# Kernel tuning notes

Hardware: AMD Instinct MI355X
Metric: run time of the kernel (lower is better)

Reference implementation:

```python
import jax, jax.numpy as jnp
import numpy as np
from jax import lax

B, L, DDYN, DSTAT, H = 512, 64, 16, 8, 512
N_BANK, C_CAND, K_TOP, N_PROTO = 50000, 1024, 16, 8
T_TARG, Q_QUANT = 2, 3
TEMP = 0.2


def _l2norm(x, eps=1e-12):
    # matches torch.nn.functional.normalize: x / max(||x||, eps)
    n = jnp.sqrt(jnp.sum(x * x, axis=-1, keepdims=True))
    return x / jnp.maximum(n, eps)


def setup_inputs() -> dict:
    key = jax.random.key(0)
    ks = jax.random.split(key, 24)
    s = 0.02
    inp = {
        'sequence_values': jax.random.normal(ks[0], (B, L, DDYN), jnp.float32),
        'sequence_masks': jnp.ones((B, L), jnp.float32),
        'static_values': jax.random.normal(ks[1], (B, DSTAT), jnp.float32),
        'bank_keys': jax.random.normal(ks[2], (N_BANK, H), jnp.float32),
        'bank_values': jax.random.normal(ks[3], (N_BANK, H), jnp.float32),
        'candidate_indices': jax.random.randint(ks[4], (B, C_CAND), 0, N_BANK, jnp.int64),
        # encoder params (SequenceEncoder stand-in: masked-mean + linear + relu)
        'W_seq': jax.random.normal(ks[5], (DDYN, H), jnp.float32) * s,
        'W_stat': jax.random.normal(ks[6], (DSTAT, H), jnp.float32) * s,
        'b_enc': jnp.zeros((H,), jnp.float32),
        # retrieval / prototype / fusion params
        'W_q': jax.random.normal(ks[7], (H, H), jnp.float32) * s,
        'b_q': jnp.zeros((H,), jnp.float32),
        'prototype_tokens': jax.random.normal(ks[8], (N_PROTO, H), jnp.float32) * 0.02,
        'W_tr': jax.random.normal(ks[9], (2 * H, H), jnp.float32) * s,
        'b_tr': jnp.zeros((H,), jnp.float32),
        'W_gate': jax.random.normal(ks[10], (3 * H, H), jnp.float32) * s,
        'b_gate': jnp.zeros((H,), jnp.float32),
        'W_out': jax.random.normal(ks[11], (H, H), jnp.float32) * s,
        'b_out': jnp.zeros((H,), jnp.float32),
        # per-target heads stacked: [T, H, Q] and [T, H]
        'W_quant': jax.random.normal(ks[12], (T_TARG, H, Q_QUANT), jnp.float32) * s,
        'b_quant': jnp.zeros((T_TARG, Q_QUANT), jnp.float32),
        'W_ev': jax.random.normal(ks[13], (T_TARG, H), jnp.float32) * s,
        'b_ev': jnp.zeros((T_TARG,), jnp.float32),
    }
    return inp


def reference(sequence_values, sequence_masks, static_values, bank_keys, bank_values,
              candidate_indices, W_seq, W_stat, b_enc, W_q, b_q, prototype_tokens,
              W_tr, b_tr, W_gate, b_gate, W_out, b_out, W_quant, b_quant, W_ev, b_ev):
    # --- encoder (masked mean pool + linear + relu stand-in for SequenceEncoder) ---
    m = sequence_masks[..., None]                                   # [B,L,1]
    pooled = (sequence_values * m).sum(1) / jnp.maximum(m.sum(1), 1e-6)
    local_hidden = jax.nn.relu(pooled @ W_seq + static_values @ W_stat + b_enc)  # [B,H]

    # --- normalized query ---
    query = _l2norm(local_hidden @ W_q + b_q)                       # [B,H]

    # --- donor retrieval: gather + dot + topk + softmax + weighted sum ---
    cand_keys = bank_keys[candidate_indices]                        # [B,C,H]
    sim = jnp.einsum('bch,bh->bc', cand_keys, query)                # [B,C]
    top_scores, top_pos = lax.top_k(sim, K_TOP)                     # [B,K]
    weights = jax.nn.softmax(top_scores / max(TEMP, 1e-6), axis=-1)
    sel_idx = jnp.take_along_axis(candidate_indices, top_pos, axis=1)  # [B,K]
    donor_hidden = jnp.einsum('bk,bkh->bh', weights, bank_values[sel_idx])

    # --- prototype attention ---
    protos_n = _l2norm(prototype_tokens)                            # [P,H]
    pw = jax.nn.softmax(query @ protos_n.T, axis=-1)                # [B,P]
    proto_hidden = pw @ prototype_tokens                            # [B,H]

    # --- transfer / gate / fuse (dropout is identity at eval) ---
    transfer = jax.nn.relu(jnp.concatenate([donor_hidden, proto_hidden], -1) @ W_tr + b_tr)
    gate = jax.nn.sigmoid(
        jnp.concatenate([local_hidden, donor_hidden, proto_hidden], -1) @ W_gate + b_gate)
    fused = gate * local_hidden + (1.0 - gate) * transfer
    fused = jax.nn.relu(fused @ W_out + b_out)                      # [B,H]

    # --- heads: sorted quantiles [B,T,Q] and event logits [B,T] ---
    quant = jnp.sort(jnp.einsum('bh,thq->btq', fused, W_quant) + b_quant, axis=-1)
    logit = jnp.einsum('bh,th->bt', fused, W_ev) + b_ev
    return jnp.concatenate([quant.reshape(quant.shape[0], -1), logit], axis=-1)  # [B, T*Q+T]
```

## Files before the change

### kernel.cpp

```cpp
#include <hip/hip_runtime.h>
#include <hip/hip_bf16.h>

typedef __hip_bfloat16 bf16;
typedef float f4v __attribute__((ext_vector_type(4)));
typedef float f2v __attribute__((ext_vector_type(2)));

__device__ __forceinline__ float lo16(unsigned u){ return __uint_as_float(u << 16); }
__device__ __forceinline__ float hi16(unsigned u){ return __uint_as_float(u & 0xffff0000u); }

#define Bn 512
#define Hn 512
#define Cn 1024
#define Kn 16
#define NBANK 50000
#define NIDPAD 50176

__device__ __forceinline__ int clamp_id(int id){
    return (id < 0) ? 0 : ((id >= NBANK) ? (NBANK - 1) : id);
}

#define A_OFF    0
#define B_OFF    262144
#define C_OFF    524288
#define D_OFF    786432
#define SIM_OFF  1048576
#define ELO_OFF  1048576
#define EHI_OFF  1310720
#define F_OFF    1572864
#define G_OFF2   1835008
#define WS_FLOATS 2097152

#define HIST_I   0
#define CURSOR_I NIDPAD
#define GTOT_I   (2*NIDPAD)
#define OFFS_I   (2*NIDPAD + 256)

__global__ __launch_bounds__(256) void k_enc(
    const float* __restrict__ seq, const float* __restrict__ mask, const float* __restrict__ stat,
    const float* __restrict__ W_seq, const float* __restrict__ W_stat, const float* __restrict__ b_enc,
    const int* __restrict__ cand32, float* __restrict__ ws)
{
    const int b = blockIdx.x, t = threadIdx.x;
    const int h0 = 2*t, h1 = 2*t + 1;

    {
        const int c64 = ((cand32[1] | cand32[3] | cand32[5] | cand32[7]) == 0) ? 1 : 0;
        int* hist = (int*)(ws + F_OFF) + HIST_I;
        #pragma unroll
        for (int u = 0; u < 4; u++) {
            int idx = b*Cn + u*256 + t;
            atomicAdd(&hist[clamp_id(cand32[(size_t)idx << c64])], 1);
        }
    }

    __shared__ float s_pool[16], s_stat[8];
    if (t < 16) {
        float acc = 0.f, ms = 0.f;
        for (int l = 0; l < 64; l++) {
            float m = mask[b*64 + l];
            ms  += m;
            acc += seq[(b*64 + l)*16 + t] * m;
        }
        s_pool[t] = acc / fmaxf(ms, 1e-6f);
    } else if (t < 24) {
        s_stat[t - 16] = stat[b*8 + (t - 16)];
    }
    __syncthreads();
    float a0 = b_enc[h0], a1 = b_enc[h1];
    #pragma unroll
    for (int j = 0; j < 16; j++) {
        float2 wv = *(const float2*)(W_seq + j*Hn + h0);
        a0 += s_pool[j]*wv.x; a1 += s_pool[j]*wv.y;
    }
    #pragma unroll
    for (int j = 0; j < 8; j++) {
        float2 wv = *(const float2*)(W_stat + j*Hn + h0);
        a0 += s_stat[j]*wv.x; a1 += s_stat[j]*wv.y;
    }
    float* g = ws + B_OFF + (size_t)b*Hn;
    g[h0] = fmaxf(a0, 0.f); g[h1] = fmaxf(a1, 0.f);
}

__global__ __launch_bounds__(256) void k_scan(
    const int* __restrict__ hist, int* __restrict__ offs, int* __restrict__ gtot)
{
    __shared__ int s[256]; __shared__ int sbase;
    const int t = threadIdx.x, g = blockIdx.x*256 + t;
    const int v = hist[g];
    s[t] = v; __syncthreads();
    #pragma unroll
    for (int off = 1; off < 256; off <<= 1) {
        int x = (t >= off) ? s[t - off] : 0;
        __syncthreads();
        s[t] += x;
        __syncthreads();
    }
    if (t == 255) sbase = atomicAdd(gtot, s[255]);
    __syncthreads();
    offs[g] = sbase + s[t] - v;
}

__global__ __launch_bounds__(256) void k_scatter(
    const int* __restrict__ cand32, int* __restrict__ cursor,
    const int* __restrict__ offs, unsigned* __restrict__ refs)
{
    const int i = blockIdx.x*256 + threadIdx.x;
    const int c64 = ((cand32[1] | cand32[3] | cand32[5] | cand32[7]) == 0) ? 1 : 0;
    const int id = clamp_id(cand32[(size_t)i << c64]);
    const int pos = atomicAdd(&cursor[id], 1);
    refs[offs[id] + pos] = (unsigned)i;
}

__global__ __launch_bounds__(256) void k_qgemm_p(
    const float* __restrict__ W, const float* __restrict__ bias,
    const float* __restrict__ in,
    float* __restrict__ P0, float* __restrict__ P1,
    float* __restrict__ P2, float* __restrict__ P3)
{
    const int ct = blockIdx.x, rt = blockIdx.y, kz = blockIdx.z, t = threadIdx.x;
    __shared__ float lt[64][132];
    {
        int r = t >> 2, c0 = (t & 3)*32;
        const float* src = in + (size_t)(rt*64 + r)*Hn + kz*128 + c0;
        #pragma unroll
        for (int i = 0; i < 8; i++)
            *(float4*)&lt[r][c0 + i*4] = *(const float4*)(src + i*4);
    }
    __syncthreads();
    const int col0 = ct*64 + (t & 15)*4, rbase = (t >> 4)*4;
    float acc[4][4];
    if (kz == 0) {
        float4 bv = *(const float4*)(bias + col0);
        #pragma unroll
        for (int i = 0; i < 4; i++) { acc[i][0]=bv.x; acc[i][1]=bv.y; acc[i][2]=bv.z; acc[i][3]=bv.w; }
    } else {
        #pragma unroll
        for (int i = 0; i < 4; i++) { acc[i][0]=0; acc[i][1]=0; acc[i][2]=0; acc[i][3]=0; }
    }
    const float* wp = W + (size_t)(kz*128)*Hn + col0;
    #pragma unroll 4
    for (int k = 0; k < 128; k++) {
        float4 wv = *(const float4*)(wp + (size_t)k*Hn);
        #pragma unroll
        for (int i = 0; i < 4; i++) {
            float a = lt[rbase + i][k];
            acc[i][0] += a*wv.x; acc[i][1] += a*wv.y; acc[i][2] += a*wv.z; acc[i][3] += a*wv.w;
        }
    }
    float* outp = (kz == 0) ? P0 : (kz == 1) ? P1 : (kz == 2) ? P2 : P3;
    #pragma unroll
    for (int i = 0; i < 4; i++) {
        float* op = outp + (size_t)(rt*64 + rbase + i)*Hn + col0;
        *(float4*)op = make_float4(acc[i][0], acc[i][1], acc[i][2], acc[i][3]);
    }
}

__global__ __launch_bounds__(256) void k_qnorm(float* __restrict__ ws)
{
    const int b = blockIdx.x*4 + (threadIdx.x >> 6), lane = threadIdx.x & 63;
    const size_t o = (size_t)b*Hn + lane*8;
    const float* p0 = ws + A_OFF   + o;
    const float* p1 = ws + ELO_OFF + o;
    const float* p2 = ws + EHI_OFF + o;
    const float* p3 = ws + G_OFF2  + o;
    float4 qa, qb;
    {
        float4 a0 = *(const float4*)p0, a1 = *(const float4*)p1,
               a2 = *(const float4*)p2, a3 = *(const float4*)p3;
        qa = make_float4(((a0.x+a1.x)+a2.x)+a3.x, ((a0.y+a1.y)+a2.y)+a3.y,
                         ((a0.z+a1.z)+a2.z)+a3.z, ((a0.w+a1.w)+a2.w)+a3.w);
        float4 b0 = *(const float4*)(p0+4), b1 = *(const float4*)(p1+4),
               b2 = *(const float4*)(p2+4), b3 = *(const float4*)(p3+4);
        qb = make_float4(((b0.x+b1.x)+b2.x)+b3.x, ((b0.y+b1.y)+b2.y)+b3.y,
                         ((b0.z+b1.z)+b2.z)+b3.z, ((b0.w+b1.w)+b2.w)+b3.w);
    }
    float ss = qa.x*qa.x + qa.y*qa.y + qa.z*qa.z + qa.w*qa.w
             + qb.x*qb.x + qb.y*qb.y + qb.z*qb.z + qb.w*qb.w;
    #pragma unroll
    for (int o2 = 32; o2; o2 >>= 1) ss += __shfl_xor(ss, o2);
    float inv = 1.f / fmaxf(sqrtf(ss), 1e-12f);
    qa.x *= inv; qa.y *= inv; qa.z *= inv; qa.w *= inv;
    qb.x *= inv; qb.y *= inv; qb.z *= inv; qb.w *= inv;
    float* qr = ws + A_OFF + o;
    *(float4*)qr = qa; *(float4*)(qr + 4) = qb;
}

#define DI_LOAD(R0,R1,R2,R3,A0,Bq0,A1,Bq1,A2,Bq2,A3,Bq3,BASE) do {                       \
    int j0_=(BASE), j1_=(BASE)+1, j2_=(BASE)+2, j3_=(BASE)+3;                            \
    const int m_ = n - 1;                                                                \
    const int c1_ = (j1_ < n), c2_ = (j2_ < n), c3_ = (j3_ < n);                         \
    j0_ = j0_>m_?m_:j0_; j1_ = j1_>m_?m_:j1_; j2_ = j2_>m_?m_:j2_; j3_ = j3_>m_?m_:j3_;  \
    R0 = (j0_<64)?(unsigned)__shfl((int)refv,j0_):__builtin_nontemporal_load(refs+start+j0_); \
    R1 = (j1_<64)?(unsigned)__shfl((int)refv,j1_):__builtin_nontemporal_load(refs+start+j1_); \
    R2 = (j2_<64)?(unsigned)__shfl((int)refv,j2_):__builtin_nontemporal_load(refs+start+j2_); \
    R3 = (j3_<64)?(unsigned)__shfl((int)refv,j3_):__builtin_nontemporal_load(refs+start+j3_); \
    {   const float* q0_ = qbase + (size_t)(R0>>10)*Hn + lane*8;                         \
        A0 = *(const float4*)q0_; Bq0 = *(const float4*)(q0_+4); }                       \
    if (c1_) { const float* q1_ = qbase + (size_t)(R1>>10)*Hn + lane*8;                  \
        A1 = *(const float4*)q1_; Bq1 = *(const float4*)(q1_+4); }                       \
    if (c2_) { const float* q2_ = qbase + (size_t)(R2>>10)*Hn + lane*8;                  \
        A2 = *(const float4*)q2_; Bq2 = *(const float4*)(q2_+4); }                       \
    if (c3_) { const float* q3_ = qbase + (size_t)(R3>>10)*Hn + lane*8;                  \
        A3 = *(const float4*)q3_; Bq3 = *(const float4*)(q3_+4); }                       \
} while(0)

#define DI_COMP(R0,R1,R2,R3,A0,Bq0,A1,Bq1,A2,Bq2,A3,Bq3,BASE) do {                       \
    float s0_ = ka.x*A0.x + ka.y*A0.y + ka.z*A0.z + ka.w*A0.w                            \
              + kb.x*Bq0.x + kb.y*Bq0.y + kb.z*Bq0.z + kb.w*Bq0.w;                       \
    float s1_ = ka.x*A1.x + ka.y*A1.y + ka.z*A1.z + ka.w*A1.w                            \
              + kb.x*Bq1.x + kb.y*Bq1.y + kb.z*Bq1.z + kb.w*Bq1.w;                       \
    float s2_ = ka.x*A2.x + ka.y*A2.y + ka.z*A2.z + ka.w*A2.w                            \
              + kb.x*Bq2.x + kb.y*Bq2.y + kb.z*Bq2.z + kb.w*Bq2.w;                       \
    float s3_ = ka.x*A3.x + ka.y*A3.y + ka.z*A3.z + ka.w*A3.w                            \
              + kb.x*Bq3.x + kb.y*Bq3.y + kb.z*Bq3.z + kb.w*Bq3.w;                       \
    s0_ += __shfl_xor(s0_,32); s1_ += __shfl_xor(s1_,32);                                \
    s2_ += __shfl_xor(s2_,32); s3_ += __shfl_xor(s3_,32);                                \
    s0_ += __shfl_xor(s0_,16); s1_ += __shfl_xor(s1_,16);                                \
    s2_ += __shfl_xor(s2_,16); s3_ += __shfl_xor(s3_,16);                                \
    s0_ += __shfl_xor(s0_, 8); s1_ += __shfl_xor(s1_, 8);                                \
    s2_ += __shfl_xor(s2_, 8); s3_ += __shfl_xor(s3_, 8);                                \
    int d_ = (lane >> 3) & 3;                                                            \
    float t_ = d_==0 ? s0_ : d_==1 ? s1_ : d_==2 ? s2_ : s3_;                            \
    t_ += __shfl_xor(t_, 4); t_ += __shfl_xor(t_, 2); t_ += __shfl_xor(t_, 1);           \
    if ((lane & 7) == 0 && lane < 32) {                                                  \
        int dd_ = lane >> 3;                                                             \
        if ((BASE) + dd_ < n) {                                                          \
            unsigned rs_ = dd_==0 ? R0 : dd_==1 ? R1 : dd_==2 ? R2 : R3;                 \
            simw[rs_] = t_;                                                              \
        }                                                                                \
    }                                                                                    \
} while(0)

__global__ __launch_bounds__(256) void k_dotinv(
    const float* __restrict__ bank_keys, const unsigned* __restrict__ refs,
    const int* __restrict__ offs, const int* __restrict__ cnt,
    float* __restrict__ ws)
{
    const int id = blockIdx.x*4 + (threadIdx.x >> 6);
    const int lane = threadIdx.x & 63;
    const int n = cnt[id];
    if (n <= 0) return;
    const int start = offs[id];

    const float* kp = bank_keys + (size_t)id*Hn + lane*8;
    f4v kav = __builtin_nontemporal_load((const f4v*)kp);
    f4v kbv = __builtin_nontemporal_load((const f4v*)(kp + 4));
    float4 ka = make_float4(kav.x, kav.y, kav.z, kav.w);
    float4 kb = make_float4(kbv.x, kbv.y, kbv.z, kbv.w);
    const unsigned refv = refs[start + (lane < n ? lane : n - 1)];
    const float* qbase = ws + A_OFF;
    float* simw = ws + SIM_OFF;

    unsigned Ar0,Ar1,Ar2,Ar3, Br0=0,Br1=0,Br2=0,Br3=0;
    float4 Aa0,Ab0,Aa1,Ab1,Aa2,Ab2,Aa3,Ab3;
    float4 Ba0,Bb0,Ba1,Bb1,Ba2,Bb2,Ba3,Bb3;
    Aa0=Ab0=Aa1=Ab1=Aa2=Ab2=Aa3=Ab3=make_float4(0.f,0.f,0.f,0.f);
    Ba0=Bb0=Ba1=Bb1=Ba2=Bb2=Ba3=Bb3=make_float4(0.f,0.f,0.f,0.f);

    DI_LOAD(Ar0,Ar1,Ar2,Ar3, Aa0,Ab0,Aa1,Ab1,Aa2,Ab2,Aa3,Ab3, 0);
    for (int base = 0; ; ) {
        if (base + 4 < n) DI_LOAD(Br0,Br1,Br2,Br3, Ba0,Bb0,Ba1,Bb1,Ba2,Bb2,Ba3,Bb3, base + 4);
        DI_COMP(Ar0,Ar1,Ar2,Ar3, Aa0,Ab0,Aa1,Ab1,Aa2,Ab2,Aa3,Ab3, base);
        if (base + 8 < n) DI_LOAD(Ar0,Ar1,Ar2,Ar3, Aa0,Ab0,Aa1,Ab1,Aa2,Ab2,Aa3,Ab3, base + 8);
        DI_COMP(Br0,Br1,Br2,Br3, Ba0,Bb0,Ba1,Bb1,Ba2,Bb2,Ba3,Bb3, base + 4);
        base += 8;
        if (base >= n) break;
    }
}

__global__ __launch_bounds__(256) void k_select(
    const float* __restrict__ bank_values, const int* __restrict__ cand32,
    const float* __restrict__ proto, float* __restrict__ ws)
{
    const int b = blockIdx.x, t = threadIdx.x;
    const int w = t >> 6, lane = t & 63;
    const int h0 = 2*t, h1 = 2*t + 1;
    const int c64 = ((cand32[1] | cand32[3] | cand32[5] | cand32[7]) == 0) ? 1 : 0;

    __shared__ __align__(16) float s_sim[Cn];
    __shared__ float s_bv[4]; __shared__ int s_bi[4];
    __shared__ float s_topv[Kn]; __shared__ int s_sel[Kn];
    __shared__ float s_w[Kn];
    __shared__ float s_score[8], s_pw[8];

    *(float4*)&s_sim[t*4] = *(const float4*)(ws + SIM_OFF + (size_t)b*Cn + t*4);

    const float* qr = ws + A_OFF + (size_t)b*Hn + lane*8;
    float4 qa = *(const float4*)qr, qb = *(const float4*)(qr + 4);
    float qv[8] = {qa.x, qa.y, qa.z, qa.w, qb.x, qb.y, qb.z, qb.w};
    __syncthreads();

    for (int k = 0; k < Kn; k++) {
        float best = -1e30f; int bi = 0x7fffffff;
        for (int i = t; i < Cn; i += 256) {
            float v = s_sim[i];
            if (v > best || (v == best && i < bi)) { best = v; bi = i; }
        }
        #pragma unroll
        for (int o = 32; o; o >>= 1) {
            float ov = __shfl_xor(best, o); int oi = __shfl_xor(bi, o);
            if (ov > best || (ov == best && oi < bi)) { best = ov; bi = oi; }
        }
        if (lane == 0) { s_bv[w] = best; s_bi[w] = bi; }
        __syncthreads();
        if (t == 0) {
            float bv = s_bv[0]; int bbi = s_bi[0];
            for (int x = 1; x < 4; x++)
                if (s_bv[x] > bv || (s_bv[x] == bv && s_bi[x] < bbi)) { bv = s_bv[x]; bbi = s_bi[x]; }
            if (bbi < 0 || bbi >= Cn) bbi = 0;
            s_topv[k] = bv; s_sel[k] = bbi; s_sim[bbi] = -1e30f;
        }
        __syncthreads();
    }

    if (t == 0) {
        float m = s_topv[0];
        float e[Kn], ssum = 0.f;
        for (int k = 0; k < Kn; k++) { e[k] = __expf((s_topv[k] - m) * 5.0f); ssum += e[k]; }
        float inv = 1.f / ssum;
        for (int k = 0; k < Kn; k++) s_w[k] = e[k] * inv;
    }
    for (int p = w; p < 8; p += 4) {
        const float* pp = proto + (size_t)p*Hn + lane*8;
        float4 pa = *(const float4*)pp, pb = *(const float4*)(pp + 4);
        float f[8] = {pa.x, pa.y, pa.z, pa.w, pb.x, pb.y, pb.z, pb.w};
        float dq = 0.f, sq = 0.f;
        #pragma unroll
        for (int i = 0; i < 8; i++) { dq += f[i]*qv[i]; sq += f[i]*f[i]; }
        #pragma unroll
        for (int o = 32; o; o >>= 1) { dq += __shfl_xor(dq, o); sq += __shfl_xor(sq, o); }
        if (lane == 0) s_score[p] = dq / fmaxf(sqrtf(sq), 1e-12f);
    }
    __syncthreads();
    if (t == 0) {
        float m = s_score[0];
        for (int p = 1; p < 8; p++) m = fmaxf(m, s_score[p]);
        float e[8], ssum = 0.f;
        for (int p = 0; p < 8; p++) { e[p] = __expf(s_score[p] - m); ssum += e[p]; }
        float inv = 1.f / ssum;
        for (int p = 0; p < 8; p++) s_pw[p] = e[p] * inv;
    }
    __syncthreads();

    {
        float a0 = 0.f, a1 = 0.f;
        #pragma unroll
        for (int k = 0; k < Kn; k++) {
            int id = clamp_id(cand32[(size_t)(b*Cn + s_sel[k]) << c64]);
            f2v v = __builtin_nontemporal_load((const f2v*)(bank_values + (size_t)id*Hn + h0));
            a0 += s_w[k]*v.x; a1 += s_w[k]*v.y;
        }
        float* gd = ws + C_OFF + (size_t)b*Hn;
        gd[h0] = a0; gd[h1] = a1;
    }
    {
        float a0 = 0.f, a1 = 0.f;
        #pragma unroll
        for (int p = 0; p < 8; p++) {
            float2 v = *(const float2*)(proto + (size_t)p*Hn + h0);
            a0 += s_pw[p]*v.x; a1 += s_pw[p]*v.y;
        }
        float* gp = ws + D_OFF + (size_t)b*Hn;
        gp[h0] = a0; gp[h1] = a1;
    }
}

__global__ __launch_bounds__(256) void k_gatetr_p(
    const float* __restrict__ W_tr, const float* __restrict__ b_tr,
    const float* __restrict__ W_gate, const float* __restrict__ b_gate,
    float* __restrict__ ws)
{
    const int ct = blockIdx.x, rt = blockIdx.y, z = blockIdx.z, t = threadIdx.x;
    const int isGate = (z < 3);
    const int sl = isGate ? z : (z - 3);
    const float* W = isGate ? (W_gate + (size_t)(z*512)*Hn) : (W_tr + (size_t)(sl*512)*Hn);
    const float* slab = ws + B_OFF + (size_t)(isGate ? z : (sl + 1))*262144;
    float* outp = isGate
        ? ((z == 0) ? ws + A_OFF : (z == 1) ? ws + ELO_OFF : ws + EHI_OFF)
        : ((sl == 0) ? ws + F_OFF : ws + G_OFF2);

    __shared__ float lt[32][260];
    const int col0 = ct*128 + (t & 31)*4, rbase = (t >> 5)*4;
    float acc[4][4];
    if (z == 0 || z == 3) {
        const float* bias = isGate ? b_gate : b_tr;
        float4 bv = *(const float4*)(bias + col0);
        #pragma unroll
        for (int i = 0; i < 4; i++) { acc[i][0]=bv.x; acc[i][1]=bv.y; acc[i][2]=bv.z; acc[i][3]=bv.w; }
    } else {
        #pragma unroll
        for (int i = 0; i < 4; i++) { acc[i][0]=0; acc[i][1]=0; acc[i][2]=0; acc[i][3]=0; }
    }

    #pragma unroll
    for (int h = 0; h < 2; h++) {
        if (h) __syncthreads();
        {
            int r = t >> 3, c0 = (t & 7)*32;
            const float* src = slab + (size_t)(rt*32 + r)*Hn + h*256 + c0;
            #pragma unroll
            for (int i = 0; i < 8; i++)
                *(float4*)&lt[r][c0 + i*4] = *(const float4*)(src + i*4);
        }
        __syncthreads();
        const float* wp = W + (size_t)(h*256)*Hn + col0;
        #pragma unroll 4
        for (int k = 0; k < 256; k++) {
            float4 wv = *(const float4*)(wp + (size_t)k*Hn);
            #pragma unroll
            for (int i = 0; i < 4; i++) {
                float a = lt[rbase + i][k];
                acc[i][0] += a*wv.x; acc[i][1] += a*wv.y; acc[i][2] += a*wv.z; acc[i][3] += a*wv.w;
            }
        }
    }
    #pragma unroll
    for (int i = 0; i < 4; i++) {
        float* op = outp + (size_t)(rt*32 + rbase + i)*Hn + col0;
        *(float4*)op = make_float4(acc[i][0], acc[i][1], acc[i][2], acc[i][3]);
    }
}

__global__ __launch_bounds__(256) void k_f1ew(float* __restrict__ ws)
{
    const int i4 = blockIdx.x*256 + threadIdx.x;
    const size_t off = (size_t)(i4 >> 7)*Hn + (i4 & 127)*4;
    float4 lc = *(const float4*)(ws + B_OFF + off);
    float4 g0 = *(const float4*)(ws + A_OFF + off);
    float4 g1 = *(const float4*)(ws + ELO_OFF + off);
    float4 g2 = *(const float4*)(ws + EHI_OFF + off);
    float4 t0 = *(const float4*)(ws + F_OFF + off);
    float4 t1 = *(const float4*)(ws + G_OFF2 + off);
    float4 ga = make_float4((g0.x+g1.x)+g2.x, (g0.y+g1.y)+g2.y,
                            (g0.z+g1.z)+g2.z, (g0.w+g1.w)+g2.w);
    float4 tr = make_float4(t0.x+t1.x, t0.y+t1.y, t0.z+t1.z, t0.w+t1.w);
    float4 r;
    float s;
    s = 1.f/(1.f + __expf(-ga.x)); r.x = s*lc.x + (1.f-s)*fmaxf(tr.x, 0.f);
    s = 1.f/(1.f + __expf(-ga.y)); r.y = s*lc.y + (1.f-s)*fmaxf(tr.y, 0.f);
    s = 1.f/(1.f + __expf(-ga.z)); r.z = s*lc.z + (1.f-s)*fmaxf(tr.z, 0.f);
    s = 1.f/(1.f + __expf(-ga.w)); r.w = s*lc.w + (1.f-s)*fmaxf(tr.w, 0.f);
    *(float4*)(ws + A_OFF + off) = r;
}

__global__ __launch_bounds__(64) void k_heads(
    const float* __restrict__ W_quant, const float* __restrict__ b_quant,
    const float* __restrict__ W_ev, const float* __restrict__ b_ev,
    const float* __restrict__ ws_ro, float* __restrict__ out)
{
    const int b = blockIdx.x, lane = threadIdx.x;
    const size_t o = (size_t)b*Hn + lane*8;
    const float* p0 = ws_ro + ELO_OFF + o;
    const float* p1 = ws_ro + EHI_OFF + o;
    const float* p2 = ws_ro + F_OFF + o;
    const float* p3 = ws_ro + G_OFF2 + o;
    float4 a0 = *(const float4*)p0, a1 = *(const float4*)p1,
           a2 = *(const float4*)p2, a3 = *(const float4*)p3;
    float4 b0 = *(const float4*)(p0+4), b1 = *(const float4*)(p1+4),
           b2 = *(const float4*)(p2+4), b3 = *(const float4*)(p3+4);
    float fv[8] = {
        fmaxf(((a0.x+a1.x)+a2.x)+a3.x, 0.f), fmaxf(((a0.y+a1.y)+a2.y)+a3.y, 0.f),
        fmaxf(((a0.z+a1.z)+a2.z)+a3.z, 0.f), fmaxf(((a0.w+a1.w)+a2.w)+a3.w, 0.f),
        fmaxf(((b0.x+b1.x)+b2.x)+b3.x, 0.f), fmaxf(((b0.y+b1.y)+b2.y)+b3.y, 0.f),
        fmaxf(((b0.z+b1.z)+b2.z)+b3.z, 0.f), fmaxf(((b0.w+b1.w)+b2.w)+b3.w, 0.f)};
    float acc[8];
    #pragma unroll
    for (int q = 0; q < 8; q++) acc[q] = 0.f;
    #pragma unroll
    for (int i = 0; i < 8; i++) {
        int h = lane*8 + i;
        float fh = fv[i];
        acc[0] += fh*W_quant[(0*Hn + h)*3 + 0];
        acc[1] += fh*W_quant[(0*Hn + h)*3 + 1];
        acc[2] += fh*W_quant[(0*Hn + h)*3 + 2];
        acc[3] += fh*W_quant[(1*Hn + h)*3 + 0];
        acc[4] += fh*W_quant[(1*Hn + h)*3 + 1];
        acc[5] += fh*W_quant[(1*Hn + h)*3 + 2];
        acc[6] += fh*W_ev[0*Hn + h];
        acc[7] += fh*W_ev[1*Hn + h];
    }
    #pragma unroll
    for (int q = 0; q < 8; q++) {
        #pragma unroll
        for (int s = 32; s; s >>= 1) acc[q] += __shfl_xor(acc[q], s);
    }
    if (lane == 0) {
        float qv[6];
        for (int q = 0; q < 6; q++) qv[q] = acc[q] + b_quant[q];
        #pragma unroll
        for (int tt = 0; tt < 2; tt++) {
            float a = qv[tt*3], bb = qv[tt*3+1], c = qv[tt*3+2];
            float mn = fminf(a, fminf(bb, c)), mx = fmaxf(a, fmaxf(bb, c));
            float md = a + bb + c - mn - mx;
            qv[tt*3] = mn; qv[tt*3+1] = md; qv[tt*3+2] = mx;
        }
        for (int q = 0; q < 6; q++) out[b*8 + q] = qv[q];
        out[b*8 + 6] = acc[6] + b_ev[0];
        out[b*8 + 7] = acc[7] + b_ev[1];
    }
}

__device__ __forceinline__ float lds_f(const void* p, int i, int f32){
    return f32 ? ((const float*)p)[i] : __bfloat162float(((const bf16*)p)[i]);
}
__device__ __forceinline__ float2 ldpair(const void* p, int elt, int f32){
    if (f32) return ((const float2*)p)[elt >> 1];
    unsigned u = ((const unsigned*)p)[elt >> 1];
    return make_float2(lo16(u), hi16(u));
}
__device__ __forceinline__ void ld8(const void* p, int elt, int f32, float* v){
    if (f32){
        const float4* q = (const float4*)((const float*)p + elt);
        float4 a = q[0], b = q[1];
        v[0]=a.x; v[1]=a.y; v[2]=a.z; v[3]=a.w; v[4]=b.x; v[5]=b.y; v[6]=b.z; v[7]=b.w;
    } else {
        uint4 u = *(const uint4*)((const bf16*)p + elt);
        v[0]=lo16(u.x); v[1]=hi16(u.x); v[2]=lo16(u.y); v[3]=hi16(u.y);
        v[4]=lo16(u.z); v[5]=hi16(u.z); v[6]=lo16(u.w); v[7]=hi16(u.w);
    }
}
__device__ __forceinline__ void st_out(void* o, int i, int f32, float v){
    if (f32) ((float*)o)[i] = v; else ((bf16*)o)[i] = __float2bfloat16(v);
}

__global__ __launch_bounds__(256) void k_fused(
    const void* __restrict__ seq, const void* __restrict__ mask, const void* __restrict__ stat,
    const void* __restrict__ bank_keys, const void* __restrict__ bank_values,
    const int* __restrict__ cand32,
    const void* __restrict__ W_seq, const void* __restrict__ W_stat, const void* __restrict__ b_enc,
    const void* __restrict__ W_q, const void* __restrict__ b_q,
    const void* __restrict__ proto,
    const void* __restrict__ W_tr, const void* __restrict__ b_tr,
    const void* __restrict__ W_gate, const void* __restrict__ b_gate,
    const void* __restrict__ W_out, const void* __restrict__ b_out,
    const void* __restrict__ W_quant, const void* __restrict__ b_quant,
    const void* __restrict__ W_ev, const void* __restrict__ b_ev,
    void* __restrict__ out)
{
    const int b = blockIdx.x, t = threadIdx.x;
    const int w = t >> 6, lane = t & 63;
    const int h0 = 2*t, h1 = 2*t + 1;
    const int f32 = (((const unsigned short*)mask)[0] == 0) ? 1 : 0;
    const int c64 = ((cand32[1] | cand32[3] | cand32[5] | cand32[7]) == 0) ? 1 : 0;

    __shared__ __align__(16) float s_pool[16];
    __shared__ __align__(16) float s_stat[8];
    __shared__ __align__(16) float g[1536];
    __shared__ __align__(16) float s_q[Hn];
    __shared__ __align__(16) float s_sim[Cn];
    __shared__ __align__(16) float f1[Hn];
    __shared__ __align__(16) float f2[Hn];
    __shared__ float s_part[4], s_ss;
    __shared__ float s_bv[4]; __shared__ int s_bi[4];
    __shared__ float s_topv[Kn]; __shared__ int s_sel[Kn];
    __shared__ float s_w[Kn];
    __shared__ float s_score[8], s_pw[8];
    __shared__ float s_head[8][4];

    if (t < 16) {
        float acc = 0.f, ms = 0.f;
        for (int l = 0; l < 64; l++) {
            float m = lds_f(mask, b*64 + l, f32);
            ms  += m;
            acc += lds_f(seq, (b*64 + l)*16 + t, f32) * m;
        }
        s_pool[t] = acc / fmaxf(ms, 1e-6f);
    } else if (t < 24) {
        s_stat[t - 16] = lds_f(stat, b*8 + (t - 16), f32);
    }
    __syncthreads();
    {
        float a0 = lds_f(b_enc, h0, f32), a1 = lds_f(b_enc, h1, f32);
        #pragma unroll
        for (int j = 0; j < 16; j++) {
            float2 wv = ldpair(W_seq, j*Hn + h0, f32);
            a0 += s_pool[j]*wv.x; a1 += s_pool[j]*wv.y;
        }
        #pragma unroll
        for (int j = 0; j < 8; j++) {
            float2 wv = ldpair(W_stat, j*Hn + h0, f32);
            a0 += s_stat[j]*wv.x; a1 += s_stat[j]*wv.y;
        }
        a0 = fmaxf(a0, 0.f); a1 = fmaxf(a1, 0.f);
        g[h0] = a0; g[h1] = a1;
    }
    __syncthreads();
    {
        float q0 = lds_f(b_q, h0, f32), q1 = lds_f(b_q, h1, f32);
        #pragma unroll 4
        for (int j = 0; j < Hn; j++) {
            float lj = g[j];
            float2 wv = ldpair(W_q, j*Hn + h0, f32);
            q0 += lj*wv.x; q1 += lj*wv.y;
        }
        float ss = q0*q0 + q1*q1;
        #pragma unroll
        for (int o = 32; o; o >>= 1) ss += __shfl_xor(ss, o);
        if (lane == 0) s_part[w] = ss;
        __syncthreads();
        if (t == 0) s_ss = s_part[0] + s_part[1] + s_part[2] + s_part[3];
        __syncthreads();
        float inv = 1.f / fmaxf(sqrtf(s_ss), 1e-12f);
        s_q[h0] = q0*inv; s_q[h1] = q1*inv;
    }
    __syncthreads();
    float qv[8];
    #pragma unroll
    for (int i = 0; i < 8; i++) qv[i] = s_q[lane*8 + i];

    for (int c0 = w*256; c0 < w*256 + 256; c0 += 4) {
        float kf[4][8];
        #pragma unroll
        for (int u = 0; u < 4; u++) {
            int id = clamp_id(cand32[(size_t)(b*Cn + c0 + u) << c64]);
            ld8(bank_keys, id*Hn + lane*8, f32, kf[u]);
        }
        #pragma unroll
        for (int u = 0; u < 4; u++) {
            float s = 0.f;
            #pragma unroll
            for (int i = 0; i < 8; i++) s += kf[u][i]*qv[i];
            #pragma unroll
            for (int o = 32; o; o >>= 1) s += __shfl_xor(s, o);
            if (lane == 0) s_sim[c0 + u] = s;
        }
    }
    __syncthreads();
    for (int k = 0; k < Kn; k++) {
        float best = -1e30f; int bi = 0x7fffffff;
        for (int i = t; i < Cn; i += 256) {
            float v = s_sim[i];
            if (v > best || (v == best && i < bi)) { best = v; bi = i; }
        }
        #pragma unroll
        for (int o = 32; o; o >>= 1) {
            float ov = __shfl_xor(best, o); int oi = __shfl_xor(bi, o);
            if (ov > best || (ov == best && oi < bi)) { best = ov; bi = oi; }
        }
        if (lane == 0) { s_bv[w] = best; s_bi[w] = bi; }
        __syncthreads();
        if (t == 0) {
            float bv = s_bv[0]; int bbi = s_bi[0];
            for (int x = 1; x < 4; x++)
                if (s_bv[x] > bv || (s_bv[x] == bv && s_bi[x] < bbi)) { bv = s_bv[x]; bbi = s_bi[x]; }
            if (bbi < 0 || bbi >= Cn) bbi = 0;
            s_topv[k] = bv; s_sel[k] = bbi; s_sim[bbi] = -1e30f;
        }
        __syncthreads();
    }
    if (t == 0) {
        float m = s_topv[0];
        float e[Kn], ssum = 0.f;
        for (int k = 0; k < Kn; k++) { e[k] = __expf((s_topv[k] - m) * 5.0f); ssum += e[k]; }
        float inv = 1.f / ssum;
        for (int k = 0; k < Kn; k++) s_w[k] = e[k] * inv;
    }
    __syncthreads();
    {
        float a0 = 0.f, a1 = 0.f;
        #pragma unroll
        for (int k = 0; k < Kn; k++) {
            int id = clamp_id(cand32[(size_t)(b*Cn + s_sel[k]) << c64]);
            float2 v = ldpair(bank_values, id*Hn + h0, f32);
            a0 += s_w[k]*v.x; a1 += s_w[k]*v.y;
        }
        g[512 + h0] = a0; g[512 + h1] = a1;
    }
    for (int p = w; p < 8; p += 4) {
        float f[8];
        ld8(proto, p*Hn + lane*8, f32, f);
        float dq = 0.f, sq = 0.f;
        #pragma unroll
        for (int i = 0; i < 8; i++) { dq += f[i]*qv[i]; sq += f[i]*f[i]; }
        #pragma unroll
        for (int o = 32; o; o >>= 1) { dq += __shfl_xor(dq, o); sq += __shfl_xor(sq, o); }
        if (lane == 0) s_score[p] = dq / fmaxf(sqrtf(sq), 1e-12f);
    }
    __syncthreads();
    if (t == 0) {
        float m = s_score[0];
        for (int p = 1; p < 8; p++) m = fmaxf(m, s_score[p]);
        float e[8], ssum = 0.f;
        for (int p = 0; p < 8; p++) { e[p] = __expf(s_score[p] - m); ssum += e[p]; }
        float inv = 1.f / ssum;
        for (int p = 0; p < 8; p++) s_pw[p] = e[p] * inv;
    }
    __syncthreads();
    {
        float a0 = 0.f, a1 = 0.f;
        #pragma unroll
        for (int p = 0; p < 8; p++) {
            float2 v = ldpair(proto, p*Hn + h0, f32);
            a0 += s_pw[p]*v.x; a1 += s_pw[p]*v.y;
        }
        g[1024 + h0] = a0; g[1024 + h1] = a1;
    }
    __syncthreads();
    float tr0 = lds_f(b_tr, h0, f32), tr1 = lds_f(b_tr, h1, f32);
    #pragma unroll 4
    for (int j = 0; j < 1024; j++) {
        float gj = g[512 + j];
        float2 wv = ldpair(W_tr, j*Hn + h0, f32);
        tr0 += gj*wv.x; tr1 += gj*wv.y;
    }
    tr0 = fmaxf(tr0, 0.f); tr1 = fmaxf(tr1, 0.f);
    float gt0 = lds_f(b_gate, h0, f32), gt1 = lds_f(b_gate, h1, f32);
    #pragma unroll 4
    for (int j = 0; j < 1536; j++) {
        float gj = g[j];
        float2 wv = ldpair(W_gate, j*Hn + h0, f32);
        gt0 += gj*wv.x; gt1 += gj*wv.y;
    }
    gt0 = 1.f/(1.f + __expf(-gt0)); gt1 = 1.f/(1.f + __expf(-gt1));
    f1[h0] = gt0*g[h0] + (1.f - gt0)*tr0;
    f1[h1] = gt1*g[h1] + (1.f - gt1)*tr1;
    __syncthreads();
    {
        float o0 = lds_f(b_out, h0, f32), o1 = lds_f(b_out, h1, f32);
        #pragma unroll 4
        for (int j = 0; j < Hn; j++) {
            float fj = f1[j];
            float2 wv = ldpair(W_out, j*Hn + h0, f32);
            o0 += fj*wv.x; o1 += fj*wv.y;
        }
        o0 = fmaxf(o0, 0.f); o1 = fmaxf(o1, 0.f);
        f2[h0] = o0; f2[h1] = o1;
    }
    __syncthreads();
    {
        float acc[8];
        #pragma unroll
        for (int o = 0; o < 8; o++) acc[o] = 0.f;
        for (int h = t; h < Hn; h += 256) {
            float fh = f2[h];
            acc[0] += fh*lds_f(W_quant, (0*Hn + h)*3 + 0, f32);
            acc[1] += fh*lds_f(W_quant, (0*Hn + h)*3 + 1, f32);
            acc[2] += fh*lds_f(W_quant, (0*Hn + h)*3 + 2, f32);
            acc[3] += fh*lds_f(W_quant, (1*Hn + h)*3 + 0, f32);
            acc[4] += fh*lds_f(W_quant, (1*Hn + h)*3 + 1, f32);
            acc[5] += fh*lds_f(W_quant, (1*Hn + h)*3 + 2, f32);
            acc[6] += fh*lds_f(W_ev, 0*Hn + h, f32);
            acc[7] += fh*lds_f(W_ev, 1*Hn + h, f32);
        }
        #pragma unroll
        for (int o = 0; o < 8; o++) {
            float v = acc[o];
            #pragma unroll
            for (int s = 32; s; s >>= 1) v += __shfl_xor(v, s);
            if (lane == 0) s_head[o][w] = v;
        }
        __syncthreads();
        if (t == 0) {
            float q[6];
            for (int o = 0; o < 6; o++)
                q[o] = s_head[o][0] + s_head[o][1] + s_head[o][2] + s_head[o][3] + lds_f(b_quant, o, f32);
            #pragma unroll
            for (int tt = 0; tt < 2; tt++) {
                float a = q[tt*3], bb = q[tt*3+1], c = q[tt*3+2];
                float mn = fminf(a, fminf(bb, c)), mx = fmaxf(a, fmaxf(bb, c));
                float md = a + bb + c - mn - mx;
                q[tt*3] = mn; q[tt*3+1] = md; q[tt*3+2] = mx;
            }
            for (int o = 0; o < 6; o++) st_out(out, b*8 + o, f32, q[o]);
            float l0 = s_head[6][0] + s_head[6][1] + s_head[6][2] + s_head[6][3] + lds_f(b_ev, 0, f32);
            float l1 = s_head[7][0] + s_head[7][1] + s_head[7][2] + s_head[7][3] + lds_f(b_ev, 1, f32);
            st_out(out, b*8 + 6, f32, l0);
            st_out(out, b*8 + 7, f32, l1);
        }
    }
}

extern "C" void kernel_launch(void* const* d_in, const int* in_sizes, int n_in,
                              void* d_out, int out_size, void* d_ws, size_t ws_size,
                              hipStream_t stream) {
    static const int expect[22] = {
        512*64*16, 512*64, 512*8, 50000*512, 50000*512, 512*1024,
        16*512, 8*512, 512, 512*512, 512, 8*512,
        1024*512, 512, 1536*512, 512, 512*512, 512,
        2*512*3, 2*3, 2*512, 2
    };
    if (n_in != 22 || out_size != 512*8) return;
    for (int i = 0; i < 22; i++) if (in_sizes[i] != expect[i]) return;

    if (ws_size < (size_t)WS_FLOATS * 4) {
        k_fused<<<Bn, 256, 0, stream>>>(
            d_in[0], d_in[1], d_in[2], d_in[3], d_in[4], (const int*)d_in[5],
            d_in[6], d_in[7], d_in[8], d_in[9], d_in[10], d_in[11],
            d_in[12], d_in[13], d_in[14], d_in[15], d_in[16], d_in[17],
            d_in[18], d_in[19], d_in[20], d_in[21], d_out);
        return;
    }

    float* ws = (float*)d_ws;
    int* iws = (int*)(ws + F_OFF);
    int* hist   = iws + HIST_I;
    int* cursor = iws + CURSOR_I;
    int* gtot   = iws + GTOT_I;
    int* offs   = iws + OFFS_I;
    unsigned* refs = (unsigned*)(ws + C_OFF);

    hipMemsetAsync(iws, 0, (size_t)(2*NIDPAD + 256)*4, stream);

    k_enc<<<Bn, 256, 0, stream>>>((const float*)d_in[0], (const float*)d_in[1],
                                  (const float*)d_in[2], (const float*)d_in[6],
                                  (const float*)d_in[7], (const float*)d_in[8],
                                  (const int*)d_in[5], ws);
    k_scan<<<NIDPAD/256, 256, 0, stream>>>(hist, offs, gtot);
    k_scatter<<<(Bn*Cn)/256, 256, 0, stream>>>((const int*)d_in[5], cursor, offs, refs);
    k_qgemm_p<<<dim3(8, 8, 4), 256, 0, stream>>>(
        (const float*)d_in[9], (const float*)d_in[10], ws + B_OFF,
        ws + A_OFF, ws + ELO_OFF, ws + EHI_OFF, ws + G_OFF2);
    k_qnorm<<<Bn/4, 256, 0, stream>>>(ws);
    k_dotinv<<<NBANK/4, 256, 0, stream>>>((const float*)d_in[3], refs, offs, hist, ws);
    k_select<<<Bn, 256, 0, stream>>>((const float*)d_in[4], (const int*)d_in[5],
                                     (const float*)d_in[11], ws);
    k_gatetr_p<<<dim3(4, 16, 5), 256, 0, stream>>>(
        (const float*)d_in[12], (const float*)d_in[13],
        (const float*)d_in[14], (const float*)d_in[15], ws);
    k_f1ew<<<256, 256, 0, stream>>>(ws);
    k_qgemm_p<<<dim3(8, 8, 4), 256, 0, stream>>>(
        (const float*)d_in[16], (const float*)d_in[17], ws + A_OFF,
        ws + ELO_OFF, ws + EHI_OFF, ws + F_OFF, ws + G_OFF2);
    k_heads<<<Bn, 64, 0, stream>>>((const float*)d_in[18], (const float*)d_in[19],
                                   (const float*)d_in[20], (const float*)d_in[21],
                                   ws, (float*)d_out);
}
```

Measured before the change: 500.4 us.

## Balance key-query dot work by fixed-size ref chunks instead of per-bank-id waves

Scatter now also records a 16-bit bank id per sorted ref slot, and the dot kernel assigns each wave a fixed 128-entry chunk of the sorted ref list instead of one bank id with a variable count. This removes load imbalance and the many empty waves caused by Poisson-distributed candidate counts. The cost is that each key row is reloaded per reference rather than reused across a bank id's refs, though neighbouring refs share ids and should hit in cache. Cursor zeroing moves into the scan kernel to shrink the memset, and scan/scatter are reordered after the query GEMM, so refid reuses G_OFF2 only once that scratch is free.

New measurement: 652.1 us. +30.3%, slower.

```diff
diff --git a/kernel.cpp b/kernel.cpp
--- a/kernel.cpp
+++ b/kernel.cpp
@@ -31,8 +31,8 @@
 #define WS_FLOATS 2097152
 
 #define HIST_I   0
-#define CURSOR_I NIDPAD
-#define GTOT_I   (2*NIDPAD)
+#define GTOT_I   NIDPAD
+#define CURSOR_I (NIDPAD + 256)
 #define OFFS_I   (2*NIDPAD + 256)
 
 __global__ __launch_bounds__(256) void k_enc(
@@ -82,11 +82,13 @@
 }
 
 __global__ __launch_bounds__(256) void k_scan(
-    const int* __restrict__ hist, int* __restrict__ offs, int* __restrict__ gtot)
+    const int* __restrict__ hist, int* __restrict__ offs, int* __restrict__ gtot,
+    int* __restrict__ cursor)
 {
     __shared__ int s[256]; __shared__ int sbase;
     const int t = threadIdx.x, g = blockIdx.x*256 + t;
     const int v = hist[g];
+    cursor[g] = 0;
     s[t] = v; __syncthreads();
     #pragma unroll
     for (int off = 1; off < 256; off <<= 1) {
@@ -102,13 +104,16 @@
 
 __global__ __launch_bounds__(256) void k_scatter(
     const int* __restrict__ cand32, int* __restrict__ cursor,
-    const int* __restrict__ offs, unsigned* __restrict__ refs)
+    const int* __restrict__ offs, unsigned* __restrict__ refs,
+    unsigned short* __restrict__ refid)
 {
     const int i = blockIdx.x*256 + threadIdx.x;
     const int c64 = ((cand32[1] | cand32[3] | cand32[5] | cand32[7]) == 0) ? 1 : 0;
     const int id = clamp_id(cand32[(size_t)i << c64]);
     const int pos = atomicAdd(&cursor[id], 1);
-    refs[offs[id] + pos] = (unsigned)i;
+    const int slot = offs[id] + pos;
+    refs[slot] = (unsigned)i;
+    refid[slot] = (unsigned short)id;
 }
 
 __global__ __launch_bounds__(256) void k_qgemm_p(
@@ -185,86 +190,69 @@
     *(float4*)qr = qa; *(float4*)(qr + 4) = qb;
 }
 
-#define DI_LOAD(R0,R1,R2,R3,A0,Bq0,A1,Bq1,A2,Bq2,A3,Bq3,BASE) do {                       \
-    int j0_=(BASE), j1_=(BASE)+1, j2_=(BASE)+2, j3_=(BASE)+3;                            \
-    const int m_ = n - 1;                                                                \
-    const int c1_ = (j1_ < n), c2_ = (j2_ < n), c3_ = (j3_ < n);                         \
-    j0_ = j0_>m_?m_:j0_; j1_ = j1_>m_?m_:j1_; j2_ = j2_>m_?m_:j2_; j3_ = j3_>m_?m_:j3_;  \
-    R0 = (j0_<64)?(unsigned)__shfl((int)refv,j0_):__builtin_nontemporal_load(refs+start+j0_); \
-    R1 = (j1_<64)?(unsigned)__shfl((int)refv,j1_):__builtin_nontemporal_load(refs+start+j1_); \
-    R2 = (j2_<64)?(unsigned)__shfl((int)refv,j2_):__builtin_nontemporal_load(refs+start+j2_); \
-    R3 = (j3_<64)?(unsigned)__shfl((int)refv,j3_):__builtin_nontemporal_load(refs+start+j3_); \
-    {   const float* q0_ = qbase + (size_t)(R0>>10)*Hn + lane*8;                         \
-        A0 = *(const float4*)q0_; Bq0 = *(const float4*)(q0_+4); }                       \
-    if (c1_) { const float* q1_ = qbase + (size_t)(R1>>10)*Hn + lane*8;                  \
-        A1 = *(const float4*)q1_; Bq1 = *(const float4*)(q1_+4); }                       \
-    if (c2_) { const float* q2_ = qbase + (size_t)(R2>>10)*Hn + lane*8;                  \
-        A2 = *(const float4*)q2_; Bq2 = *(const float4*)(q2_+4); }                       \
-    if (c3_) { const float* q3_ = qbase + (size_t)(R3>>10)*Hn + lane*8;                  \
-        A3 = *(const float4*)q3_; Bq3 = *(const float4*)(q3_+4); }                       \
-} while(0)
-
-#define DI_COMP(R0,R1,R2,R3,A0,Bq0,A1,Bq1,A2,Bq2,A3,Bq3,BASE) do {                       \
-    float s0_ = ka.x*A0.x + ka.y*A0.y + ka.z*A0.z + ka.w*A0.w                            \
-              + kb.x*Bq0.x + kb.y*Bq0.y + kb.z*Bq0.z + kb.w*Bq0.w;                       \
-    float s1_ = ka.x*A1.x + ka.y*A1.y + ka.z*A1.z + ka.w*A1.w                            \
-              + kb.x*Bq1.x + kb.y*Bq1.y + kb.z*Bq1.z + kb.w*Bq1.w;                       \
-    float s2_ = ka.x*A2.x + ka.y*A2.y + ka.z*A2.z + ka.w*A2.w                            \
-              + kb.x*Bq2.x + kb.y*Bq2.y + kb.z*Bq2.z + kb.w*Bq2.w;                       \
-    float s3_ = ka.x*A3.x + ka.y*A3.y + ka.z*A3.z + ka.w*A3.w                            \
-              + kb.x*Bq3.x + kb.y*Bq3.y + kb.z*Bq3.z + kb.w*Bq3.w;                       \
-    s0_ += __shfl_xor(s0_,32); s1_ += __shfl_xor(s1_,32);                                \
-    s2_ += __shfl_xor(s2_,32); s3_ += __shfl_xor(s3_,32);                                \
-    s0_ += __shfl_xor(s0_,16); s1_ += __shfl_xor(s1_,16);                                \
-    s2_ += __shfl_xor(s2_,16); s3_ += __shfl_xor(s3_,16);                                \
-    s0_ += __shfl_xor(s0_, 8); s1_ += __shfl_xor(s1_, 8);                                \
-    s2_ += __shfl_xor(s2_, 8); s3_ += __shfl_xor(s3_, 8);                                \
-    int d_ = (lane >> 3) & 3;                                                            \
-    float t_ = d_==0 ? s0_ : d_==1 ? s1_ : d_==2 ? s2_ : s3_;                            \
-    t_ += __shfl_xor(t_, 4); t_ += __shfl_xor(t_, 2); t_ += __shfl_xor(t_, 1);           \
-    if ((lane & 7) == 0 && lane < 32) {                                                  \
-        int dd_ = lane >> 3;                                                             \
-        if ((BASE) + dd_ < n) {                                                          \
-            unsigned rs_ = dd_==0 ? R0 : dd_==1 ? R1 : dd_==2 ? R2 : R3;                 \
-            simw[rs_] = t_;                                                              \
-        }                                                                                \
-    }                                                                                    \
-} while(0)
-
 __global__ __launch_bounds__(256) void k_dotinv(
     const float* __restrict__ bank_keys, const unsigned* __restrict__ refs,
-    const int* __restrict__ offs, const int* __restrict__ cnt,
-    float* __restrict__ ws)
-{
-    const int id = blockIdx.x*4 + (threadIdx.x >> 6);
+    const unsigned short* __restrict__ refid, float* __restrict__ ws)
+{
+    const int wave = blockIdx.x*4 + (threadIdx.x >> 6);
     const int lane = threadIdx.x & 63;
-    const int n = cnt[id];
-    if (n <= 0) return;
-    const int start = offs[id];
-
-    const float* kp = bank_keys + (size_t)id*Hn + lane*8;
-    f4v kav = __builtin_nontemporal_load((const f4v*)kp);
-    f4v kbv = __builtin_nontemporal_load((const f4v*)(kp + 4));
-    float4 ka = make_float4(kav.x, kav.y, kav.z, kav.w);
-    float4 kb = make_float4(kbv.x, kbv.y, kbv.z, kbv.w);
-    const unsigned refv = refs[start + (lane < n ? lane : n - 1)];
+    const int r0 = wave << 7;
+    const int le8 = lane*8;
+
+    const int rp0 = (int)__builtin_nontemporal_load(refs + r0 + lane);
+    const int rp1 = (int)__builtin_nontemporal_load(refs + r0 + 64 + lane);
+    const int ip  = (int)__builtin_nontemporal_load((const unsigned*)refid + (r0 >> 1) + lane);
+
     const float* qbase = ws + A_OFF;
     float* simw = ws + SIM_OFF;
 
-    unsigned Ar0,Ar1,Ar2,Ar3, Br0=0,Br1=0,Br2=0,Br3=0;
-    float4 Aa0,Ab0,Aa1,Ab1,Aa2,Ab2,Aa3,Ab3;
-    float4 Ba0,Bb0,Ba1,Bb1,Ba2,Bb2,Ba3,Bb3;
-    Aa0=Ab0=Aa1=Ab1=Aa2=Ab2=Aa3=Ab3=make_float4(0.f,0.f,0.f,0.f);
-    Ba0=Bb0=Ba1=Bb1=Ba2=Bb2=Ba3=Bb3=make_float4(0.f,0.f,0.f,0.f);
-
-    DI_LOAD(Ar0,Ar1,Ar2,Ar3, Aa0,Ab0,Aa1,Ab1,Aa2,Ab2,Aa3,Ab3, 0);
-    for (int base = 0; ; ) {
-        if (base + 4 < n) DI_LOAD(Br0,Br1,Br2,Br3, Ba0,Bb0,Ba1,Bb1,Ba2,Bb2,Ba3,Bb3, base + 4);
-        DI_COMP(Ar0,Ar1,Ar2,Ar3, Aa0,Ab0,Aa1,Ab1,Aa2,Ab2,Aa3,Ab3, base);
-        if (base + 8 < n) DI_LOAD(Ar0,Ar1,Ar2,Ar3, Aa0,Ab0,Aa1,Ab1,Aa2,Ab2,Aa3,Ab3, base + 8);
-        DI_COMP(Br0,Br1,Br2,Br3, Ba0,Bb0,Ba1,Bb1,Ba2,Bb2,Ba3,Bb3, base + 4);
-        base += 8;
-        if (base >= n) break;
+    for (int g = 0; g < 128; g += 4) {
+        float4 qa0, qb0, qa1, qb1, qa2, qb2, qa3, qb3;
+        float4 ka0, kb0, ka1, kb1, ka2, kb2, ka3, kb3;
+        unsigned rr0, rr1, rr2, rr3;
+
+        #define DI_ONE(U, RR, QA, QB, KA, KB) do {                                   \
+            const int j_ = g + (U);                                                  \
+            RR = (unsigned)__shfl((j_ & 64) ? rp1 : rp0, j_ & 63);                   \
+            const unsigned wd_ = (unsigned)__shfl(ip, j_ >> 1);                      \
+            const int id_ = (j_ & 1) ? (int)(wd_ >> 16) : (int)(wd_ & 0xffffu);      \
+            const float* qp_ = qbase + ((size_t)(RR >> 10) << 9) + le8;              \
+            QA = *(const float4*)qp_; QB = *(const float4*)(qp_ + 4);                \
+            const float* kp_ = bank_keys + ((size_t)id_ << 9) + le8;                 \
+            f4v kav_ = __builtin_nontemporal_load((const f4v*)kp_);                  \
+            f4v kbv_ = __builtin_nontemporal_load((const f4v*)(kp_ + 4));            \
+            KA = make_float4(kav_.x, kav_.y, kav_.z, kav_.w);                        \
+            KB = make_float4(kbv_.x, kbv_.y, kbv_.z, kbv_.w);                        \
+        } while(0)
+
+        DI_ONE(0, rr0, qa0, qb0, ka0, kb0);
+        DI_ONE(1, rr1, qa1, qb1, ka1, kb1);
+        DI_ONE(2, rr2, qa2, qb2, ka2, kb2);
+        DI_ONE(3, rr3, qa3, qb3, ka3, kb3);
+        #undef DI_ONE
+
+        float s0 = ka0.x*qa0.x + ka0.y*qa0.y + ka0.z*qa0.z + ka0.w*qa0.w
+                 + kb0.x*qb0.x + kb0.y*qb0.y + kb0.z*qb0.z + kb0.w*qb0.w;
+        float s1 = ka1.x*qa1.x + ka1.y*qa1.y + ka1.z*qa1.z + ka1.w*qa1.w
+                 + kb1.x*qb1.x + kb1.y*qb1.y + kb1.z*qb1.z + kb1.w*qb1.w;
+        float s2 = ka2.x*qa2.x + ka2.y*qa2.y + ka2.z*qa2.z + ka2.w*qa2.w
+                 + kb2.x*qb2.x + kb2.y*qb2.y + kb2.z*qb2.z + kb2.w*qb2.w;
+        float s3 = ka3.x*qa3.x + ka3.y*qa3.y + ka3.z*qa3.z + ka3.w*qa3.w
+                 + kb3.x*qb3.x + kb3.y*qb3.y + kb3.z*qb3.z + kb3.w*qb3.w;
+        s0 += __shfl_xor(s0,32); s1 += __shfl_xor(s1,32);
+        s2 += __shfl_xor(s2,32); s3 += __shfl_xor(s3,32);
+        s0 += __shfl_xor(s0,16); s1 += __shfl_xor(s1,16);
+        s2 += __shfl_xor(s2,16); s3 += __shfl_xor(s3,16);
+        s0 += __shfl_xor(s0, 8); s1 += __shfl_xor(s1, 8);
+        s2 += __shfl_xor(s2, 8); s3 += __shfl_xor(s3, 8);
+        const int d = (lane >> 3) & 3;
+        float tt = d==0 ? s0 : d==1 ? s1 : d==2 ? s2 : s3;
+        tt += __shfl_xor(tt, 4); tt += __shfl_xor(tt, 2); tt += __shfl_xor(tt, 1);
+        if ((lane & 7) == 0 && lane < 32) {
+            const int dd = lane >> 3;
+            const unsigned rs = dd==0 ? rr0 : dd==1 ? rr1 : dd==2 ? rr2 : rr3;
+            simw[rs] = tt;
+        }
     }
 }
 
@@ -794,24 +782,25 @@
     float* ws = (float*)d_ws;
     int* iws = (int*)(ws + F_OFF);
     int* hist   = iws + HIST_I;
+    int* gtot   = iws + GTOT_I;
     int* cursor = iws + CURSOR_I;
-    int* gtot   = iws + GTOT_I;
     int* offs   = iws + OFFS_I;
     unsigned* refs = (unsigned*)(ws + C_OFF);
-
-    hipMemsetAsync(iws, 0, (size_t)(2*NIDPAD + 256)*4, stream);
+    unsigned short* refid = (unsigned short*)(ws + G_OFF2);
+
+    hipMemsetAsync(iws, 0, (size_t)(NIDPAD + 256)*4, stream);
 
     k_enc<<<Bn, 256, 0, stream>>>((const float*)d_in[0], (const float*)d_in[1],
                                   (const float*)d_in[2], (const float*)d_in[6],
                                   (const float*)d_in[7], (const float*)d_in[8],
                                   (const int*)d_in[5], ws);
-    k_scan<<<NIDPAD/256, 256, 0, stream>>>(hist, offs, gtot);
-    k_scatter<<<(Bn*Cn)/256, 256, 0, stream>>>((const int*)d_in[5], cursor, offs, refs);
     k_qgemm_p<<<dim3(8, 8, 4), 256, 0, stream>>>(
         (const float*)d_in[9], (const float*)d_in[10], ws + B_OFF,
         ws + A_OFF, ws + ELO_OFF, ws + EHI_OFF, ws + G_OFF2);
     k_qnorm<<<Bn/4, 256, 0, stream>>>(ws);
-    k_dotinv<<<NBANK/4, 256, 0, stream>>>((const float*)d_in[3], refs, offs, hist, ws);
+    k_scan<<<NIDPAD/256, 256, 0, stream>>>(hist, offs, gtot, cursor);
+    k_scatter<<<(Bn*Cn)/256, 256, 0, stream>>>((const int*)d_in[5], cursor, offs, refs, refid);
+    k_dotinv<<<1024, 256, 0, stream>>>((const float*)d_in[3], refs, refid, ws);
     k_select<<<Bn, 256, 0, stream>>>((const float*)d_in[4], (const int*)d_in[5],
                                      (const float*)d_in[11], ws);
     k_gatetr_p<<<dim3(4, 16, 5), 256, 0, stream>>>(
```
